# Performance work log

Measured on AMD Instinct MI355X. Metric: run time of the kernel, lower is better.

The kernel has to match this reference:

```python
import jax, jax.numpy as jnp
import numpy as np


def setup_inputs() -> dict:
    key = jax.random.key(0)
    k1, k2, k3 = jax.random.split(key, 3)
    B, E, S = 8, 2048, 2048
    x = jax.random.normal(k1, (B, E, S), dtype=jnp.float32)
    weight = jax.random.normal(k2, (1, S), dtype=jnp.float32)
    diag_weight = jax.random.normal(k3, (1, S), dtype=jnp.float32)
    bias = jnp.zeros((S,), dtype=jnp.float32)
    decay_value = jnp.ones((2, 1), dtype=jnp.float32)
    return {"x": x, "weight": weight, "diag_weight": diag_weight,
            "bias": bias, "decay_value": decay_value}


def _build_matrix(weight, diag_weight, decay_value):
    # Upper-triangular (strict) decay matrix M[i,j] = v[i] * d**(j-i) for j>i,
    # plus diagonal M[j,j] = v2[j].  d = clip(decay_value[1], 0.9, 1.0).
    v = weight.reshape(-1)       # (S,)
    v2 = diag_weight.reshape(-1)  # (S,)
    S = v.shape[0]
    idx = jnp.arange(S)
    diff = idx[None, :] - idx[:, None]          # j - i, shape (S, S)
    d = jnp.clip(decay_value[1, 0], 0.9, 1.0)   # scalar
    strict_upper = jnp.where(diff > 0, v[:, None] * d ** diff, jnp.zeros((), dtype=v.dtype))
    return strict_upper + jnp.diag(v2)          # (S, S)


def reference(x, weight, diag_weight, bias, decay_value):
    # x: (B, E, S); mixes along the sequence axis with the causal-decay matrix.
    M = _build_matrix(weight, diag_weight, decay_value)
    out = jnp.einsum('bes,st->bet', x, M) + bias  # bias broadcasts over last (seq) dim
    return out
```

## Files before the change

kernel.cpp:

```cpp
#include <hip/hip_runtime.h>


#define SEQ 2048
#define THREADS 512
#define ROWS_PER_BLOCK 8

__global__ __launch_bounds__(THREADS, 8) void decay_scan_kernel(
    const float* __restrict__ x,
    const float* __restrict__ weight,
    const float* __restrict__ diag_weight,
    const float* __restrict__ bias,
    const float* __restrict__ decay,
    float* __restrict__ out)
{
    const int tid  = threadIdx.x;
    const int lane = tid & 63;
    const int wv   = tid >> 6;
    const int off  = tid * 4;
    const long base = (long)blockIdx.x * ROWS_PER_BLOCK * SEQ;

    const float d = fminf(fmaxf(decay[1], 0.9f), 1.0f);
    const float d2 = d * d, d3 = d2 * d;

    float dq[7];
    dq[0] = d2 * d2;
    #pragma unroll
    for (int k = 1; k < 7; ++k) dq[k] = dq[k - 1] * dq[k - 1];
    const float d256 = dq[6];
    float dpow = 1.f;
    #pragma unroll
    for (int k = 0; k < 6; ++k) if ((lane >> k) & 1) dpow *= dq[k];

    const float4 vv = *(const float4*)(weight + off);
    const float4 gv = *(const float4*)(diag_weight + off);
    const float4 bv = *(const float4*)(bias + off);

    __shared__ float ws[2][8];

    float4 xv = *(const float4*)(x + base + off);

    #pragma unroll
    for (int r = 0; r < ROWS_PER_BLOCK; ++r) {
        float4 xn;
        if (r + 1 < ROWS_PER_BLOCK)
            xn = *(const float4*)(x + base + (long)(r + 1) * SEQ + off);

        const float xa[4] = {xv.x, xv.y, xv.z, xv.w};

        float lp1, lp2, lp3;
        float c;
        c = d * (xa[0] * vv.x);            lp1 = c;
        c = d * fmaf(xa[1], vv.y, c);      lp2 = c;
        c = d * fmaf(xa[2], vv.z, c);      lp3 = c;
        c = d * fmaf(xa[3], vv.w, c);

        float s = c;
        #pragma unroll
        for (int k = 0; k < 6; ++k) {
            const int o = 1 << k;
            const float s2 = __shfl_up(s, o, 64);
            if (lane >= o) s = fmaf(s2, dq[k], s);
        }
        float es = __shfl_up(s, 1, 64);
        if (lane == 0) es = 0.f;

        if (lane == 63) ws[r & 1][wv] = s;
        __syncthreads();
        float cs = 0.f;
        const float* wrow = ws[r & 1];
        #pragma unroll
        for (int w = 0; w < 7; ++w) {
            if (w < wv) cs = fmaf(cs, d256, wrow[w]);
        }
        const float C = fmaf(cs, dpow, es);

        float4 o4;
        o4.x = fmaf(xa[0], gv.x, C                + bv.x);
        o4.y = fmaf(xa[1], gv.y, fmaf(C, d,  lp1) + bv.y);
        o4.z = fmaf(xa[2], gv.z, fmaf(C, d2, lp2) + bv.z);
        o4.w = fmaf(xa[3], gv.w, fmaf(C, d3, lp3) + bv.w);
        *(float4*)(out + base + (long)r * SEQ + off) = o4;

        xv = xn;
    }
}

extern "C" void kernel_launch(void* const* d_in, const int* in_sizes, int n_in,
                              void* d_out, int out_size, void* d_ws, size_t ws_size,
                              hipStream_t stream) {
    const float* x           = (const float*)d_in[0];
    const float* weight      = (const float*)d_in[1];
    const float* diag_weight = (const float*)d_in[2];
    const float* bias        = (const float*)d_in[3];
    const float* decay       = (const float*)d_in[4];
    float* out = (float*)d_out;

    const int rows = in_sizes[0] / SEQ;
    decay_scan_kernel<<<rows / ROWS_PER_BLOCK, THREADS, 0, stream>>>(
        x, weight, diag_weight, bias, decay, out);
}
```

Baseline: 242.1 us.

## Batch four rows per scan step to share barriers and interleave shuffles

Processes rows in groups of four. The wavefront shuffle scans for the four rows are interleaved, and all four rows share a single __syncthreads, so there are two barriers per block instead of eight. Loads for the next group of four rows are issued ahead of time. This aims to hide shuffle latency through ILP and cut synchronisation overhead, at the cost of more registers per thread; the launch_bounds occupancy hint is dropped to allow for that.

```diff
diff --git a/kernel.cpp b/kernel.cpp
--- a/kernel.cpp
+++ b/kernel.cpp
@@ -3,9 +3,11 @@
 
 #define SEQ 2048
 #define THREADS 512
-#define ROWS_PER_BLOCK 8
+#define G 4
+#define NGROUPS 2
+#define ROWS_PER_BLOCK (G * NGROUPS)
 
-__global__ __launch_bounds__(THREADS, 8) void decay_scan_kernel(
+__global__ __launch_bounds__(THREADS) void decay_scan_kernel(
     const float* __restrict__ x,
     const float* __restrict__ weight,
     const float* __restrict__ diag_weight,
@@ -22,11 +24,11 @@
     const float d = fminf(fmaxf(decay[1], 0.9f), 1.0f);
     const float d2 = d * d, d3 = d2 * d;
 
-    float dq[7];
+    float dq[6];
     dq[0] = d2 * d2;
     #pragma unroll
-    for (int k = 1; k < 7; ++k) dq[k] = dq[k - 1] * dq[k - 1];
-    const float d256 = dq[6];
+    for (int k = 1; k < 6; ++k) dq[k] = dq[k - 1] * dq[k - 1];
+    const float d256 = dq[5] * dq[5];
     float dpow = 1.f;
     #pragma unroll
     for (int k = 0; k < 6; ++k) if ((lane >> k) & 1) dpow *= dq[k];
@@ -35,53 +37,74 @@
     const float4 gv = *(const float4*)(diag_weight + off);
     const float4 bv = *(const float4*)(bias + off);
 
-    __shared__ float ws[2][8];
+    __shared__ float ws[NGROUPS][G][8];
 
-    float4 xv = *(const float4*)(x + base + off);
+    float4 xv[G];
+    #pragma unroll
+    for (int r = 0; r < G; ++r)
+        xv[r] = *(const float4*)(x + base + (long)r * SEQ + off);
 
     #pragma unroll
-    for (int r = 0; r < ROWS_PER_BLOCK; ++r) {
-        float4 xn;
-        if (r + 1 < ROWS_PER_BLOCK)
-            xn = *(const float4*)(x + base + (long)(r + 1) * SEQ + off);
+    for (int grp = 0; grp < NGROUPS; ++grp) {
+        float4 xn[G];
+        if (grp + 1 < NGROUPS) {
+            #pragma unroll
+            for (int r = 0; r < G; ++r)
+                xn[r] = *(const float4*)(x + base + (long)((grp + 1) * G + r) * SEQ + off);
+        }
 
-        const float xa[4] = {xv.x, xv.y, xv.z, xv.w};
+        float lp1[G], lp2[G], lp3[G], s[G];
+        #pragma unroll
+        for (int r = 0; r < G; ++r) {
+            float c;
+            c = d * (xv[r].x * vv.x);        lp1[r] = c;
+            c = d * fmaf(xv[r].y, vv.y, c);  lp2[r] = c;
+            c = d * fmaf(xv[r].z, vv.z, c);  lp3[r] = c;
+            c = d * fmaf(xv[r].w, vv.w, c);
+            s[r] = c;
+        }
 
-        float lp1, lp2, lp3;
-        float c;
-        c = d * (xa[0] * vv.x);            lp1 = c;
-        c = d * fmaf(xa[1], vv.y, c);      lp2 = c;
-        c = d * fmaf(xa[2], vv.z, c);      lp3 = c;
-        c = d * fmaf(xa[3], vv.w, c);
-
-        float s = c;
         #pragma unroll
         for (int k = 0; k < 6; ++k) {
             const int o = 1 << k;
-            const float s2 = __shfl_up(s, o, 64);
-            if (lane >= o) s = fmaf(s2, dq[k], s);
+            float t[G];
+            #pragma unroll
+            for (int r = 0; r < G; ++r) t[r] = __shfl_up(s[r], o, 64);
+            #pragma unroll
+            for (int r = 0; r < G; ++r) if (lane >= o) s[r] = fmaf(t[r], dq[k], s[r]);
         }
-        float es = __shfl_up(s, 1, 64);
-        if (lane == 0) es = 0.f;
+        float es[G];
+        #pragma unroll
+        for (int r = 0; r < G; ++r) {
+            es[r] = __shfl_up(s[r], 1, 64);
+            if (lane == 0) es[r] = 0.f;
+        }
 
-        if (lane == 63) ws[r & 1][wv] = s;
+        if (lane == 63) {
+            #pragma unroll
+            for (int r = 0; r < G; ++r) ws[grp][r][wv] = s[r];
+        }
         __syncthreads();
-        float cs = 0.f;
-        const float* wrow = ws[r & 1];
+
         #pragma unroll
-        for (int w = 0; w < 7; ++w) {
-            if (w < wv) cs = fmaf(cs, d256, wrow[w]);
+        for (int r = 0; r < G; ++r) {
+            float cs = 0.f;
+            #pragma unroll
+            for (int w = 0; w < 7; ++w)
+                if (w < wv) cs = fmaf(cs, d256, ws[grp][r][w]);
+            const float C = fmaf(cs, dpow, es[r]);
+            float4 o4;
+            o4.x = fmaf(xv[r].x, gv.x, C                   + bv.x);
+            o4.y = fmaf(xv[r].y, gv.y, fmaf(C, d,  lp1[r]) + bv.y);
+            o4.z = fmaf(xv[r].z, gv.z, fmaf(C, d2, lp2[r]) + bv.z);
+            o4.w = fmaf(xv[r].w, gv.w, fmaf(C, d3, lp3[r]) + bv.w);
+            *(float4*)(out + base + (long)(grp * G + r) * SEQ + off) = o4;
         }
-        const float C = fmaf(cs, dpow, es);
 
-        float4 o4;
-        o4.x = fmaf(xa[0], gv.x, C                + bv.x);
-        o4.y = fmaf(xa[1], gv.y, fmaf(C, d,  lp1) + bv.y);
-        o4.z = fmaf(xa[2], gv.z, fmaf(C, d2, lp2) + bv.z);
-        o4.w = fmaf(xa[3], gv.w, fmaf(C, d3, lp3) + bv.w);
-        *(float4*)(out + base + (long)r * SEQ + off) = o4;
-
-        xv = xn;
+        if (grp + 1 < NGROUPS) {
+            #pragma unroll
+            for (int r = 0; r < G; ++r) xv[r] = xn[r];
+        }
     }
 }
 
```

Measured after the change: 239.4 us. Within noise of the previous version (-1.1%).
